# Kernel optimization log

Hardware: AMD Instinct MI355X
Metric: run time of the kernel (lower is better)

Reference implementation:

```python
import jax, jax.numpy as jnp
import numpy as np

EMBED_DIM = 1024
NUM_HEADS = 16
HEAD_DIM = EMBED_DIM // NUM_HEADS


def setup_inputs() -> dict:
    key = jax.random.key(0)
    ks = jax.random.split(key, 9)
    B, S, D = 4, 2048, EMBED_DIM
    s = 1.0 / np.sqrt(D)
    return {
        "x": jax.random.normal(ks[0], (B, S, D), dtype=jnp.float32),
        "Wq": jax.random.uniform(ks[1], (D, D), jnp.float32, -s, s),
        "bq": jax.random.uniform(ks[2], (D,), jnp.float32, -s, s),
        "Wk": jax.random.uniform(ks[3], (D, D), jnp.float32, -s, s),
        "bk": jax.random.uniform(ks[4], (D,), jnp.float32, -s, s),
        "Wv": jax.random.uniform(ks[5], (D, D), jnp.float32, -s, s),
        "bv": jax.random.uniform(ks[6], (D,), jnp.float32, -s, s),
        "Wo": jax.random.uniform(ks[7], (D, D), jnp.float32, -s, s),
        "bo": jax.random.uniform(ks[8], (D,), jnp.float32, -s, s),
    }


def reference(x, Wq, bq, Wk, bk, Wv, bv, Wo, bo):
    B, S, D = x.shape
    H, Hd = NUM_HEADS, HEAD_DIM

    def proj(W, b):
        # torch Linear: x @ W.T + b; reshape to [B, H, S, Hd]
        y = jnp.einsum('bsd,ed->bse', x, W) + b
        return y.reshape(B, S, H, Hd).transpose(0, 2, 1, 3)

    Q = proj(Wq, bq)
    K = proj(Wk, bk)
    V = proj(Wv, bv)
    scores = jnp.einsum('bhqd,bhkd->bhqk', Q, K) / np.sqrt(Hd).astype(jnp.float32)
    attn = jax.nn.softmax(scores, axis=-1)
    out = jnp.einsum('bhqk,bhkd->bhqd', attn, V)
    out = out.transpose(0, 2, 1, 3).reshape(B, S, D)
    return jnp.einsum('bsd,ed->bse', out, Wo) + bo
```

## Files before the change

### kernel.cpp

```cpp
#include <hip/hip_runtime.h>
#include <stdint.h>

typedef unsigned short u16;
typedef _Float16 f16;
typedef __fp16 fp16x2 __attribute__((ext_vector_type(2)));
typedef f16 f16x4 __attribute__((ext_vector_type(4)));
typedef f16 f16x8 __attribute__((ext_vector_type(8)));
typedef float f32x4 __attribute__((ext_vector_type(4)));
typedef u16 u16x8v __attribute__((ext_vector_type(8)));
typedef uint32_t u32x4 __attribute__((ext_vector_type(4)));

#define MFMAH  __builtin_amdgcn_mfma_f32_16x16x32_f16

__device__ __forceinline__ void gload16(const void* g, void* l) {
    __builtin_amdgcn_global_load_lds(
        (const __attribute__((address_space(1))) uint32_t*)g,
        (__attribute__((address_space(3))) uint32_t*)l, 16, 0, 0);
}

__global__ __launch_bounds__(256) void convert_x(const float4* __restrict__ x,
                                                 f16x8* __restrict__ o) {
    int i = blockIdx.x * 256 + threadIdx.x;
    float4 a = x[2 * i], b = x[2 * i + 1];
    f16x8 h;
    h[0] = (f16)a.x; h[1] = (f16)a.y; h[2] = (f16)a.z; h[3] = (f16)a.w;
    h[4] = (f16)b.x; h[5] = (f16)b.y; h[6] = (f16)b.z; h[7] = (f16)b.w;
    o[i] = h;
}

__global__ __launch_bounds__(256) void convert_w(const float4* __restrict__ Wq,
                                                 const float4* __restrict__ Wk,
                                                 const float4* __restrict__ Wv,
                                                 const float4* __restrict__ Wo,
                                                 f16x8* __restrict__ hi,
                                                 f16x8* __restrict__ lo) {
    int gi = blockIdx.x * 256 + threadIdx.x;
    int wsel = gi >> 17;
    int li = gi & 131071;
    const float4* src = (wsel == 0) ? Wq : (wsel == 1) ? Wk : (wsel == 2) ? Wv : Wo;
    float4 a = src[2 * li], b = src[2 * li + 1];
    float v[8] = {a.x, a.y, a.z, a.w, b.x, b.y, b.z, b.w};
    f16x8 h;
#pragma unroll
    for (int j = 0; j < 8; ++j) h[j] = (f16)v[j];
    hi[gi] = h;
    if (wsel == 3) {
        f16x8 l;
#pragma unroll
        for (int j = 0; j < 8; ++j) l[j] = (f16)(v[j] - (float)h[j]);
        lo[gi] = l;
    }
}

__global__ __launch_bounds__(512, 4)
void gemm_qkv(const f16* __restrict__ A,
              const f16* __restrict__ Whi,
              const float* __restrict__ b0, const float* __restrict__ b1,
              const float* __restrict__ b2,
              f16* __restrict__ oq, f16* __restrict__ ok, f16* __restrict__ ov) {
    __shared__ f16 ldsA[256 * 64];
    __shared__ f16 ldsW[128 * 64];
    const int t = threadIdx.x;
    const int lane = t & 63, quad = lane >> 4, l16 = lane & 15;
    const int wid = t >> 6;
    const int wsel = blockIdx.x >> 3;
    const int bm = blockIdx.y * 256;
    const int bn = (blockIdx.x & 7) * 128;
    const int wm = (wid >> 1) * 64, wn = (wid & 1) * 64;
    const f16* Wh = Whi + (size_t)wsel * 1048576;
    const float* bias = (wsel == 0) ? b0 : (wsel == 1) ? b1 : b2;

    f32x4 acc[4][4] = {};

    for (int kt = 0; kt < 16; ++kt) {
        __syncthreads();
        const int k0 = kt * 64;
#pragma unroll
        for (int c = 0; c < 4; ++c) {
            const int u = c * 512 + t;
            const int r = u >> 3, cc = u & 7;
            const int sc = cc ^ (r & 7);
            gload16(A + (size_t)(bm + r) * 1024 + k0 + sc * 8, &ldsA[u * 8]);
        }
#pragma unroll
        for (int c = 0; c < 2; ++c) {
            const int u = c * 512 + t;
            const int r = u >> 3, cc = u & 7;
            const int sc = cc ^ (r & 7);
            gload16(Wh + (size_t)(bn + r) * 1024 + k0 + sc * 8, &ldsW[u * 8]);
        }
        __syncthreads();

#pragma unroll
        for (int kq = 0; kq < 2; ++kq) {
            f16x8 bh[4];
            const int ch = (kq * 4 + quad) ^ (l16 & 7);
#pragma unroll
            for (int i = 0; i < 4; ++i) {
                const int rb = wn + i * 16 + l16;
                bh[i] = *(const f16x8*)&ldsW[rb * 64 + ch * 8];
            }
#pragma unroll
            for (int mi = 0; mi < 4; ++mi) {
                const int ra = wm + mi * 16 + l16;
                const f16x8 af = *(const f16x8*)&ldsA[ra * 64 + ch * 8];
#pragma unroll
                for (int ni = 0; ni < 4; ++ni)
                    acc[mi][ni] = MFMAH(af, bh[ni], acc[mi][ni], 0, 0, 0);
            }
        }
    }

#pragma unroll
    for (int ni = 0; ni < 4; ++ni) {
        const int e = bn + wn + ni * 16 + l16;
        const float bv = bias[e];
        const int h = e >> 6, d = e & 63;
#pragma unroll
        for (int mi = 0; mi < 4; ++mi) {
            const int row0 = bm + wm + mi * 16 + quad * 4;
            if (wsel == 2) {
                const int b = row0 >> 11, s0 = row0 & 2047;
                ushort4 pk;
                f16 p0 = (f16)(acc[mi][ni][0] + bv);
                f16 p1 = (f16)(acc[mi][ni][1] + bv);
                f16 p2 = (f16)(acc[mi][ni][2] + bv);
                f16 p3 = (f16)(acc[mi][ni][3] + bv);
                pk.x = __builtin_bit_cast(u16, p0);
                pk.y = __builtin_bit_cast(u16, p1);
                pk.z = __builtin_bit_cast(u16, p2);
                pk.w = __builtin_bit_cast(u16, p3);
                *(ushort4*)(ov + ((size_t)((b * 16 + h) * 64 + d)) * 2048 + s0) = pk;
            } else {
                f16* dst = (wsel == 0) ? oq : ok;
#pragma unroll
                for (int r = 0; r < 4; ++r) {
                    const int row = row0 + r;
                    const int b = row >> 11, s = row & 2047;
                    float v = acc[mi][ni][r] + bv;
                    if (wsel == 0) v *= 0.18033688f;
                    dst[((size_t)((b * 16 + h) * 2048 + s)) * 64 + d] = (f16)v;
                }
            }
        }
    }
}

__global__ __launch_bounds__(256, 2)
void gemm_o(const f16* __restrict__ A,
            const f16* __restrict__ Wh, const f16* __restrict__ Wl,
            const float* __restrict__ bias, float* __restrict__ ofp) {
    __shared__ f16 ldsA[128 * 64];
    __shared__ f16 ldsW[2][128 * 64];
    const int t = threadIdx.x;
    const int lane = t & 63, quad = lane >> 4, l16 = lane & 15;
    const int wid = t >> 6;
    const int bm = blockIdx.y * 128, bn = blockIdx.x * 128;
    const int wm = (wid >> 1) * 64, wn = (wid & 1) * 64;

    f32x4 acc[4][4] = {};

    for (int kt = 0; kt < 16; ++kt) {
        __syncthreads();
        const int k0 = kt * 64;
#pragma unroll
        for (int c = 0; c < 4; ++c) {
            const int u = c * 256 + t;
            const int r = u >> 3, cc = u & 7;
            const int sc = cc ^ (r & 7);
            gload16(A + (size_t)(bm + r) * 1024 + k0 + sc * 8, &ldsA[u * 8]);
        }
#pragma unroll
        for (int p = 0; p < 2; ++p) {
            const f16* Ws = p ? Wl : Wh;
#pragma unroll
            for (int c = 0; c < 4; ++c) {
                const int u = c * 256 + t;
                const int r = u >> 3, cc = u & 7;
                const int sc = cc ^ (r & 7);
                gload16(Ws + (size_t)(bn + r) * 1024 + k0 + sc * 8, &ldsW[p][u * 8]);
            }
        }
        __syncthreads();

#pragma unroll
        for (int kq = 0; kq < 2; ++kq) {
            f16x8 bh[4], bl[4];
            const int ch = (kq * 4 + quad) ^ (l16 & 7);
#pragma unroll
            for (int i = 0; i < 4; ++i) {
                const int rb = wn + i * 16 + l16;
                bh[i] = *(const f16x8*)&ldsW[0][rb * 64 + ch * 8];
                bl[i] = *(const f16x8*)&ldsW[1][rb * 64 + ch * 8];
            }
#pragma unroll
            for (int mi = 0; mi < 4; ++mi) {
                const int ra = wm + mi * 16 + l16;
                const f16x8 af = *(const f16x8*)&ldsA[ra * 64 + ch * 8];
#pragma unroll
                for (int ni = 0; ni < 4; ++ni) {
                    acc[mi][ni] = MFMAH(af, bh[ni], acc[mi][ni], 0, 0, 0);
                    acc[mi][ni] = MFMAH(af, bl[ni], acc[mi][ni], 0, 0, 0);
                }
            }
        }
    }

#pragma unroll
    for (int ni = 0; ni < 4; ++ni) {
        const int e = bn + wn + ni * 16 + l16;
        const float bv = bias[e];
#pragma unroll
        for (int mi = 0; mi < 4; ++mi) {
            const int row0 = bm + wm + mi * 16 + quad * 4;
#pragma unroll
            for (int r = 0; r < 4; ++r)
                ofp[(size_t)(row0 + r) * 1024 + e] = acc[mi][ni][r] + bv;
        }
    }
}

__global__ __launch_bounds__(512, 4)
void attn_fused(const f16* __restrict__ Q, const f16* __restrict__ K,
                const f16* __restrict__ Vt, f16* __restrict__ AO) {
    __shared__ f16 Kt[2][128 * 64];
    __shared__ f16 Vs[2][64 * 128];
    const int t = threadIdx.x, wid = t >> 6, lane = t & 63;
    const int quad = lane >> 4, l16 = lane & 15;
    const int sw7 = l16 & 7;
    const int bh = blockIdx.x;
    const int q0 = blockIdx.y * 256;
    const size_t base = (size_t)bh * (2048 * 64);

    const u16x8v ou = {0x3C00, 0x3C00, 0x3C00, 0x3C00, 0x3C00, 0x3C00, 0x3C00, 0x3C00};
    const f16x8 ONES8 = __builtin_bit_cast(f16x8, ou);

    f16x8 qf[2][2];
#pragma unroll
    for (int s = 0; s < 2; ++s) {
        const int qrow = q0 + wid * 32 + s * 16 + l16;
        qf[s][0] = *(const f16x8*)(Q + base + (size_t)qrow * 64 + quad * 8);
        qf[s][1] = *(const f16x8*)(Q + base + (size_t)qrow * 64 + 32 + quad * 8);
    }

    f32x4 of[2][4] = {};
    f32x4 rs[2] = {};

    auto STAGE = [&](int bf, int kt) {
#pragma unroll
        for (int c = 0; c < 2; ++c) {
            const int u = c * 512 + t;
            const int row = u >> 3, cc = u & 7;
            const int sc = cc ^ (row & 7);
            gload16(K + base + (size_t)(kt * 128 + row) * 64 + sc * 8, &Kt[bf][u * 8]);
        }
#pragma unroll
        for (int c = 0; c < 2; ++c) {
            const int u = c * 512 + t;
            const int row = u >> 4, cc = u & 15;
            const int sc = cc ^ (row & 15);
            gload16(Vt + base + (size_t)row * 2048 + kt * 128 + sc * 8, &Vs[bf][u * 8]);
        }
    };

    STAGE(0, 0);
    __syncthreads();

    for (int kt = 0; kt < 16; ++kt) {
        const int bf = kt & 1;
        if (kt < 15) STAGE(bf ^ 1, kt + 1);

#pragma unroll
        for (int kk = 0; kk < 4; ++kk) {
            u32x4 pws[2];
#pragma unroll
            for (int nn = 0; nn < 2; ++nn) {
                const int krow = (kk * 2 + nn) * 16 + l16;
                const f16x8 kb0 = *(const f16x8*)&Kt[bf][krow * 64 + (quad ^ sw7) * 8];
                const f16x8 kb1 = *(const f16x8*)&Kt[bf][krow * 64 + ((4 | quad) ^ sw7) * 8];
#pragma unroll
                for (int s = 0; s < 2; ++s) {
                    f32x4 sf = {};
                    sf = MFMAH(kb0, qf[s][0], sf, 0, 0, 0);
                    sf = MFMAH(kb1, qf[s][1], sf, 0, 0, 0);
                    const float p0 = __builtin_amdgcn_exp2f(sf[0]);
                    const float p1 = __builtin_amdgcn_exp2f(sf[1]);
                    const float p2 = __builtin_amdgcn_exp2f(sf[2]);
                    const float p3 = __builtin_amdgcn_exp2f(sf[3]);
                    pws[s][nn * 2 + 0] = __builtin_bit_cast(uint32_t, __builtin_amdgcn_cvt_pkrtz(p0, p1));
                    pws[s][nn * 2 + 1] = __builtin_bit_cast(uint32_t, __builtin_amdgcn_cvt_pkrtz(p2, p3));
                }
            }
            f16x8 pf8[2];
#pragma unroll
            for (int s = 0; s < 2; ++s)
                pf8[s] = __builtin_bit_cast(f16x8, pws[s]);

            __builtin_amdgcn_s_setprio(1);
#pragma unroll
            for (int di = 0; di < 4; ++di) {
                const int row = di * 16 + l16;
                const int col0 = kk * 32 + quad * 4;
                const int ch0 = (col0 >> 3) ^ (row & 15);
                const f16x4 v0 = *(const f16x4*)&Vs[bf][row * 128 + ch0 * 8 + (quad & 1) * 4];
                const int col1 = col0 + 16;
                const int ch1 = (col1 >> 3) ^ (row & 15);
                const f16x4 v1 = *(const f16x4*)&Vs[bf][row * 128 + ch1 * 8 + (quad & 1) * 4];
                const f16x8 vb8 = __builtin_shufflevector(v0, v1, 0, 1, 2, 3, 4, 5, 6, 7);
#pragma unroll
                for (int s = 0; s < 2; ++s)
                    of[s][di] = MFMAH(vb8, pf8[s], of[s][di], 0, 0, 0);
            }
#pragma unroll
            for (int s = 0; s < 2; ++s)
                rs[s] = MFMAH(ONES8, pf8[s], rs[s], 0, 0, 0);
            __builtin_amdgcn_s_setprio(0);
        }
        __syncthreads();
    }

    const int b = bh >> 4, h = bh & 15;
#pragma unroll
    for (int s = 0; s < 2; ++s) {
        const int qrow = q0 + wid * 32 + s * 16 + l16;
        const float inv = 1.0f / rs[s][0];
#pragma unroll
        for (int di = 0; di < 4; ++di) {
            const int e0 = h * 64 + di * 16 + quad * 4;
            ushort4 pk;
            f16 o0 = (f16)(of[s][di][0] * inv);
            f16 o1 = (f16)(of[s][di][1] * inv);
            f16 o2 = (f16)(of[s][di][2] * inv);
            f16 o3 = (f16)(of[s][di][3] * inv);
            pk.x = __builtin_bit_cast(u16, o0);
            pk.y = __builtin_bit_cast(u16, o1);
            pk.z = __builtin_bit_cast(u16, o2);
            pk.w = __builtin_bit_cast(u16, o3);
            *(ushort4*)(AO + (size_t)(b * 2048 + qrow) * 1024 + e0) = pk;
        }
    }
}

extern "C" void kernel_launch(void* const* d_in, const int* in_sizes, int n_in,
                              void* d_out, int out_size, void* d_ws, size_t ws_size,
                              hipStream_t stream) {
    const float* x  = (const float*)d_in[0];
    const float* Wq = (const float*)d_in[1];
    const float* bq = (const float*)d_in[2];
    const float* Wk = (const float*)d_in[3];
    const float* bk = (const float*)d_in[4];
    const float* Wv = (const float*)d_in[5];
    const float* bv = (const float*)d_in[6];
    const float* Wo = (const float*)d_in[7];
    const float* bo = (const float*)d_in[8];
    float* out = (float*)d_out;

    char* ws = (char*)d_ws;
    f16* XF  = (f16*)(ws);
    f16* WH  = (f16*)(ws + (16u << 20));
    f16* WL  = (f16*)(ws + (24u << 20));
    f16* QF  = (f16*)(ws + (32u << 20));
    f16* KF  = (f16*)(ws + (48u << 20));
    f16* VTF = (f16*)(ws + (64u << 20));
    f16* AOF = (f16*)(ws + (80u << 20));

    convert_x<<<4096, 256, 0, stream>>>((const float4*)x, (f16x8*)XF);
    convert_w<<<2048, 256, 0, stream>>>((const float4*)Wq, (const float4*)Wk,
                                        (const float4*)Wv, (const float4*)Wo,
                                        (f16x8*)WH, (f16x8*)WL);

    gemm_qkv<<<dim3(24, 32), 512, 0, stream>>>(XF, WH, bq, bk, bv, QF, KF, VTF);

    attn_fused<<<dim3(64, 8), 512, 0, stream>>>(QF, KF, VTF, AOF);

    gemm_o<<<dim3(8, 64), 256, 0, stream>>>(AOF, WH + 3145728, WL + 3145728, bo, out);
}
```

Measured before the change: 272.8 us.

## Double-buffer LDS in QKV and output GEMMs and merge conversion kernels

Both projection GEMMs now split the K loop into 32-wide steps with two LDS buffers, so the global-to-LDS loads for the next step are issued before the MFMAs on the current step and only one barrier is needed per step. The XOR swizzle is adapted to the narrower 32-element rows. The two fp32-to-fp16 conversion kernels are merged into one launch, and gemm_o's occupancy hint is raised from 2 to 3 blocks per CU. Halving the K tile doubles the number of barriers and loop iterations, and the higher occupancy hint may force register spills.

After: 282.4 us. 1.04x slower.

```diff
diff --git a/kernel.cpp b/kernel.cpp
--- a/kernel.cpp
+++ b/kernel.cpp
@@ -18,37 +18,39 @@
         (__attribute__((address_space(3))) uint32_t*)l, 16, 0, 0);
 }
 
-__global__ __launch_bounds__(256) void convert_x(const float4* __restrict__ x,
-                                                 f16x8* __restrict__ o) {
-    int i = blockIdx.x * 256 + threadIdx.x;
-    float4 a = x[2 * i], b = x[2 * i + 1];
-    f16x8 h;
-    h[0] = (f16)a.x; h[1] = (f16)a.y; h[2] = (f16)a.z; h[3] = (f16)a.w;
-    h[4] = (f16)b.x; h[5] = (f16)b.y; h[6] = (f16)b.z; h[7] = (f16)b.w;
-    o[i] = h;
-}
-
-__global__ __launch_bounds__(256) void convert_w(const float4* __restrict__ Wq,
-                                                 const float4* __restrict__ Wk,
-                                                 const float4* __restrict__ Wv,
-                                                 const float4* __restrict__ Wo,
-                                                 f16x8* __restrict__ hi,
-                                                 f16x8* __restrict__ lo) {
-    int gi = blockIdx.x * 256 + threadIdx.x;
-    int wsel = gi >> 17;
-    int li = gi & 131071;
-    const float4* src = (wsel == 0) ? Wq : (wsel == 1) ? Wk : (wsel == 2) ? Wv : Wo;
-    float4 a = src[2 * li], b = src[2 * li + 1];
-    float v[8] = {a.x, a.y, a.z, a.w, b.x, b.y, b.z, b.w};
-    f16x8 h;
-#pragma unroll
-    for (int j = 0; j < 8; ++j) h[j] = (f16)v[j];
-    hi[gi] = h;
-    if (wsel == 3) {
-        f16x8 l;
-#pragma unroll
-        for (int j = 0; j < 8; ++j) l[j] = (f16)(v[j] - (float)h[j]);
-        lo[gi] = l;
+__global__ __launch_bounds__(256) void convert_all(const float4* __restrict__ x,
+                                                   const float4* __restrict__ Wq,
+                                                   const float4* __restrict__ Wk,
+                                                   const float4* __restrict__ Wv,
+                                                   const float4* __restrict__ Wo,
+                                                   f16x8* __restrict__ xo,
+                                                   f16x8* __restrict__ hi,
+                                                   f16x8* __restrict__ lo) {
+    const int bid = blockIdx.x;
+    if (bid < 4096) {
+        int i = bid * 256 + threadIdx.x;
+        float4 a = x[2 * i], b = x[2 * i + 1];
+        f16x8 h;
+        h[0] = (f16)a.x; h[1] = (f16)a.y; h[2] = (f16)a.z; h[3] = (f16)a.w;
+        h[4] = (f16)b.x; h[5] = (f16)b.y; h[6] = (f16)b.z; h[7] = (f16)b.w;
+        xo[i] = h;
+    } else {
+        int gi = (bid - 4096) * 256 + threadIdx.x;
+        int wsel = gi >> 17;
+        int li = gi & 131071;
+        const float4* src = (wsel == 0) ? Wq : (wsel == 1) ? Wk : (wsel == 2) ? Wv : Wo;
+        float4 a = src[2 * li], b = src[2 * li + 1];
+        float v[8] = {a.x, a.y, a.z, a.w, b.x, b.y, b.z, b.w};
+        f16x8 h;
+#pragma unroll
+        for (int j = 0; j < 8; ++j) h[j] = (f16)v[j];
+        hi[gi] = h;
+        if (wsel == 3) {
+            f16x8 l;
+#pragma unroll
+            for (int j = 0; j < 8; ++j) l[j] = (f16)(v[j] - (float)h[j]);
+            lo[gi] = l;
+        }
     }
 }
 
@@ -58,8 +60,8 @@
               const float* __restrict__ b0, const float* __restrict__ b1,
               const float* __restrict__ b2,
               f16* __restrict__ oq, f16* __restrict__ ok, f16* __restrict__ ov) {
-    __shared__ f16 ldsA[256 * 64];
-    __shared__ f16 ldsW[128 * 64];
+    __shared__ f16 ldsA[2][256 * 32];
+    __shared__ f16 ldsW[2][128 * 32];
     const int t = threadIdx.x;
     const int lane = t & 63, quad = lane >> 4, l16 = lane & 15;
     const int wid = t >> 6;
@@ -72,43 +74,46 @@
 
     f32x4 acc[4][4] = {};
 
-    for (int kt = 0; kt < 16; ++kt) {
-        __syncthreads();
-        const int k0 = kt * 64;
-#pragma unroll
-        for (int c = 0; c < 4; ++c) {
-            const int u = c * 512 + t;
-            const int r = u >> 3, cc = u & 7;
-            const int sc = cc ^ (r & 7);
-            gload16(A + (size_t)(bm + r) * 1024 + k0 + sc * 8, &ldsA[u * 8]);
-        }
+    auto STAGE = [&](int bf, int kt) {
+        const int k0 = kt * 32;
 #pragma unroll
         for (int c = 0; c < 2; ++c) {
             const int u = c * 512 + t;
-            const int r = u >> 3, cc = u & 7;
-            const int sc = cc ^ (r & 7);
-            gload16(Wh + (size_t)(bn + r) * 1024 + k0 + sc * 8, &ldsW[u * 8]);
+            const int r = u >> 2, cc = u & 3;
+            const int sc = cc ^ ((r >> 1) & 3);
+            gload16(A + (size_t)(bm + r) * 1024 + k0 + sc * 8, &ldsA[bf][u * 8]);
+        }
+        {
+            const int u = t;
+            const int r = u >> 2, cc = u & 3;
+            const int sc = cc ^ ((r >> 1) & 3);
+            gload16(Wh + (size_t)(bn + r) * 1024 + k0 + sc * 8, &ldsW[bf][u * 8]);
+        }
+    };
+
+    STAGE(0, 0);
+    __syncthreads();
+
+    for (int kt = 0; kt < 32; ++kt) {
+        const int bf = kt & 1;
+        if (kt < 31) STAGE(bf ^ 1, kt + 1);
+
+        const int ch = quad ^ ((l16 >> 1) & 3);
+        f16x8 bh[4];
+#pragma unroll
+        for (int i = 0; i < 4; ++i) {
+            const int rb = wn + i * 16 + l16;
+            bh[i] = *(const f16x8*)&ldsW[bf][rb * 32 + ch * 8];
+        }
+#pragma unroll
+        for (int mi = 0; mi < 4; ++mi) {
+            const int ra = wm + mi * 16 + l16;
+            const f16x8 af = *(const f16x8*)&ldsA[bf][ra * 32 + ch * 8];
+#pragma unroll
+            for (int ni = 0; ni < 4; ++ni)
+                acc[mi][ni] = MFMAH(af, bh[ni], acc[mi][ni], 0, 0, 0);
         }
         __syncthreads();
-
-#pragma unroll
-        for (int kq = 0; kq < 2; ++kq) {
-            f16x8 bh[4];
-            const int ch = (kq * 4 + quad) ^ (l16 & 7);
-#pragma unroll
-            for (int i = 0; i < 4; ++i) {
-                const int rb = wn + i * 16 + l16;
-                bh[i] = *(const f16x8*)&ldsW[rb * 64 + ch * 8];
-            }
-#pragma unroll
-            for (int mi = 0; mi < 4; ++mi) {
-                const int ra = wm + mi * 16 + l16;
-                const f16x8 af = *(const f16x8*)&ldsA[ra * 64 + ch * 8];
-#pragma unroll
-                for (int ni = 0; ni < 4; ++ni)
-                    acc[mi][ni] = MFMAH(af, bh[ni], acc[mi][ni], 0, 0, 0);
-            }
-        }
     }
 
 #pragma unroll
@@ -146,12 +151,12 @@
     }
 }
 
-__global__ __launch_bounds__(256, 2)
+__global__ __launch_bounds__(256, 3)
 void gemm_o(const f16* __restrict__ A,
             const f16* __restrict__ Wh, const f16* __restrict__ Wl,
             const float* __restrict__ bias, float* __restrict__ ofp) {
-    __shared__ f16 ldsA[128 * 64];
-    __shared__ f16 ldsW[2][128 * 64];
+    __shared__ f16 ldsA[2][128 * 32];
+    __shared__ f16 ldsW[2][2][128 * 32];
     const int t = threadIdx.x;
     const int lane = t & 63, quad = lane >> 4, l16 = lane & 15;
     const int wid = t >> 6;
@@ -160,50 +165,54 @@
 
     f32x4 acc[4][4] = {};
 
-    for (int kt = 0; kt < 16; ++kt) {
-        __syncthreads();
-        const int k0 = kt * 64;
-#pragma unroll
-        for (int c = 0; c < 4; ++c) {
+    auto STAGE = [&](int bf, int kt) {
+        const int k0 = kt * 32;
+#pragma unroll
+        for (int c = 0; c < 2; ++c) {
             const int u = c * 256 + t;
-            const int r = u >> 3, cc = u & 7;
-            const int sc = cc ^ (r & 7);
-            gload16(A + (size_t)(bm + r) * 1024 + k0 + sc * 8, &ldsA[u * 8]);
+            const int r = u >> 2, cc = u & 3;
+            const int sc = cc ^ ((r >> 1) & 3);
+            gload16(A + (size_t)(bm + r) * 1024 + k0 + sc * 8, &ldsA[bf][u * 8]);
         }
 #pragma unroll
         for (int p = 0; p < 2; ++p) {
             const f16* Ws = p ? Wl : Wh;
 #pragma unroll
-            for (int c = 0; c < 4; ++c) {
+            for (int c = 0; c < 2; ++c) {
                 const int u = c * 256 + t;
-                const int r = u >> 3, cc = u & 7;
-                const int sc = cc ^ (r & 7);
-                gload16(Ws + (size_t)(bn + r) * 1024 + k0 + sc * 8, &ldsW[p][u * 8]);
+                const int r = u >> 2, cc = u & 3;
+                const int sc = cc ^ ((r >> 1) & 3);
+                gload16(Ws + (size_t)(bn + r) * 1024 + k0 + sc * 8, &ldsW[bf][p][u * 8]);
+            }
+        }
+    };
+
+    STAGE(0, 0);
+    __syncthreads();
+
+    for (int kt = 0; kt < 32; ++kt) {
+        const int bf = kt & 1;
+        if (kt < 31) STAGE(bf ^ 1, kt + 1);
+
+        const int ch = quad ^ ((l16 >> 1) & 3);
+        f16x8 bh[4], bl[4];
+#pragma unroll
+        for (int i = 0; i < 4; ++i) {
+            const int rb = wn + i * 16 + l16;
+            bh[i] = *(const f16x8*)&ldsW[bf][0][rb * 32 + ch * 8];
+            bl[i] = *(const f16x8*)&ldsW[bf][1][rb * 32 + ch * 8];
+        }
+#pragma unroll
+        for (int mi = 0; mi < 4; ++mi) {
+            const int ra = wm + mi * 16 + l16;
+            const f16x8 af = *(const f16x8*)&ldsA[bf][ra * 32 + ch * 8];
+#pragma unroll
+            for (int ni = 0; ni < 4; ++ni) {
+                acc[mi][ni] = MFMAH(af, bh[ni], acc[mi][ni], 0, 0, 0);
+                acc[mi][ni] = MFMAH(af, bl[ni], acc[mi][ni], 0, 0, 0);
             }
         }
         __syncthreads();
-
-#pragma unroll
-        for (int kq = 0; kq < 2; ++kq) {
-            f16x8 bh[4], bl[4];
-            const int ch = (kq * 4 + quad) ^ (l16 & 7);
-#pragma unroll
-            for (int i = 0; i < 4; ++i) {
-                const int rb = wn + i * 16 + l16;
-                bh[i] = *(const f16x8*)&ldsW[0][rb * 64 + ch * 8];
-                bl[i] = *(const f16x8*)&ldsW[1][rb * 64 + ch * 8];
-            }
-#pragma unroll
-            for (int mi = 0; mi < 4; ++mi) {
-                const int ra = wm + mi * 16 + l16;
-                const f16x8 af = *(const f16x8*)&ldsA[ra * 64 + ch * 8];
-#pragma unroll
-                for (int ni = 0; ni < 4; ++ni) {
-                    acc[mi][ni] = MFMAH(af, bh[ni], acc[mi][ni], 0, 0, 0);
-                    acc[mi][ni] = MFMAH(af, bl[ni], acc[mi][ni], 0, 0, 0);
-                }
-            }
-        }
     }
 
 #pragma unroll
@@ -364,10 +373,10 @@
     f16* VTF = (f16*)(ws + (64u << 20));
     f16* AOF = (f16*)(ws + (80u << 20));
 
-    convert_x<<<4096, 256, 0, stream>>>((const float4*)x, (f16x8*)XF);
-    convert_w<<<2048, 256, 0, stream>>>((const float4*)Wq, (const float4*)Wk,
-                                        (const float4*)Wv, (const float4*)Wo,
-                                        (f16x8*)WH, (f16x8*)WL);
+    convert_all<<<6144, 256, 0, stream>>>((const float4*)x,
+                                          (const float4*)Wq, (const float4*)Wk,
+                                          (const float4*)Wv, (const float4*)Wo,
+                                          (f16x8*)XF, (f16x8*)WH, (f16x8*)WL);
 
     gemm_qkv<<<dim3(24, 32), 512, 0, stream>>>(XF, WH, bq, bk, bv, QF, KF, VTF);
 
```
